# Kernel tuning notes

Hardware: AMD Instinct MI355X
Metric: run time of the kernel (lower is better)

Reference implementation:

```python
import jax, jax.numpy as jnp
import numpy as np

N_NODES = 50000
N_EDGES = 400000
IN_NODE = 16
OUT_NODE = 20
IN_EDGE = 10
HIDDEN_EDGE = 64
HIDDEN_ACTOR = 256
N_ACTIONS = 16
N_GRAPHS = 128
BN_EPS = 1e-5


def setup_inputs() -> dict:
    key = jax.random.key(0)
    ks = jax.random.split(key, 16)
    inp = {
        "x": jax.random.normal(ks[0], (N_NODES, IN_NODE), dtype=jnp.float32),
        "edge_index": jax.random.randint(ks[1], (2, N_EDGES), 0, N_NODES, dtype=jnp.int64),
        "edge_attr": jax.random.normal(ks[2], (N_EDGES, IN_EDGE), dtype=jnp.float32),
        "batch": jnp.sort(jax.random.randint(ks[3], (N_NODES,), 0, N_GRAPHS, dtype=jnp.int64)),
        # edge-nn params: Lin(in_edge,64) -> BN(64) -> ReLU -> Lin(64, in*out)
        "W1": jax.random.normal(ks[4], (IN_EDGE, HIDDEN_EDGE), dtype=jnp.float32) / np.sqrt(IN_EDGE),
        "b1": jnp.zeros((HIDDEN_EDGE,), dtype=jnp.float32),
        "gamma": jnp.ones((HIDDEN_EDGE,), dtype=jnp.float32),
        "beta": jnp.zeros((HIDDEN_EDGE,), dtype=jnp.float32),
        "W2": jax.random.normal(ks[5], (HIDDEN_EDGE, IN_NODE * OUT_NODE), dtype=jnp.float32) / np.sqrt(HIDDEN_EDGE),
        "b2": jnp.zeros((IN_NODE * OUT_NODE,), dtype=jnp.float32),
        # NNConv root weight + bias
        "root": jax.random.normal(ks[6], (IN_NODE, OUT_NODE), dtype=jnp.float32) / np.sqrt(IN_NODE),
        "bias": jnp.zeros((OUT_NODE,), dtype=jnp.float32),
        # actor MLP: Lin(20,256) -> ReLU -> Lin(256, n_actions)
        "A1": jax.random.normal(ks[7], (OUT_NODE, HIDDEN_ACTOR), dtype=jnp.float32) / np.sqrt(OUT_NODE),
        "ab1": jnp.zeros((HIDDEN_ACTOR,), dtype=jnp.float32),
        "A2": jax.random.normal(ks[8], (HIDDEN_ACTOR, N_ACTIONS), dtype=jnp.float32) / np.sqrt(HIDDEN_ACTOR),
        "ab2": jnp.zeros((N_ACTIONS,), dtype=jnp.float32),
    }
    return inp


def reference(x, edge_index, edge_attr, batch, W1, b1, gamma, beta, W2, b2, root, bias, A1, ab1, A2, ab2):
    # edge nn: Linear -> BatchNorm1d (training-mode batch stats) -> ReLU -> Linear
    h = edge_attr @ W1 + b1                                  # [E, 64]
    mu = jnp.mean(h, axis=0)
    var = jnp.mean((h - mu) ** 2, axis=0)                    # biased var, as BN uses
    h = gamma * (h - mu) * jax.lax.rsqrt(var + BN_EPS) + beta
    h = jax.nn.relu(h)
    w = (h @ W2 + b2).reshape(-1, IN_NODE, OUT_NODE)         # [E, in, out]

    src, dst = edge_index[0], edge_index[1]
    msg = jnp.einsum('ei,eio->eo', x[src], w)                # per-edge matvec, [E, out]
    agg = jax.ops.segment_sum(msg, dst, num_segments=N_NODES)  # scatter-add to targets
    out = agg + x @ root + bias                              # [N, out]

    # global_mean_pool over graphs
    sums = jax.ops.segment_sum(out, batch, num_segments=N_GRAPHS)
    counts = jax.ops.segment_sum(jnp.ones((out.shape[0],), out.dtype), batch, num_segments=N_GRAPHS)
    pooled = sums / jnp.maximum(counts, 1.0)[:, None]        # [G, out]

    a = jax.nn.relu(pooled @ A1 + ab1)
    return a @ A2 + ab2                                      # [G, n_actions]
```

## Files before the change

kernel.cpp:

```cpp
#include <hip/hip_runtime.h>

#define N_NODES   50000
#define N_EDGES   400000
#define IN_NODE   16
#define OUT_NODE  20
#define IN_EDGE   10
#define HE        64
#define HA        256
#define N_ACT     16
#define N_GRAPHS  128
#define BN_EPS    1e-5f
#define HNST      68
#define SPLIT     16

typedef __attribute__((ext_vector_type(8))) short short8v;
typedef __attribute__((ext_vector_type(4))) float f32x4;

__device__ __forceinline__ unsigned short f2bf(float f) {
  unsigned u = __float_as_uint(f);
  u += 0x7fffu + ((u >> 16) & 1u);
  return (unsigned short)(u >> 16);
}
__device__ __forceinline__ float bf2f(short s) {
  return __uint_as_float(((unsigned)(unsigned short)s) << 16);
}

#define DPP_ROR_ADD(v, CTRL)                                                  \
  ((v) + __int_as_float(__builtin_amdgcn_update_dpp(                          \
             0, __float_as_int(v), (CTRL), 0xF, 0xF, true)))
#define ROW_SUM16(v)                                                          \
  do {                                                                        \
    v = DPP_ROR_ADD(v, 0x128);                                                \
    v = DPP_ROR_ADD(v, 0x124);                                                \
    v = DPP_ROR_ADD(v, 0x122);                                                \
    v = DPP_ROR_ADD(v, 0x121);                                                \
  } while (0)

__global__ void zero_k(float* __restrict__ ws) {
  ws[blockIdx.x * 256 + threadIdx.x] = 0.f;
}

__global__ __launch_bounds__(256) void prep_k(const int* __restrict__ ei,
                                              const int* __restrict__ batch,
                                              int* __restrict__ hist) {
  __shared__ int lh[N_GRAPHS];
  const int tid = threadIdx.x;
  if (tid < N_GRAPHS) lh[tid] = 0;
  __syncthreads();
  for (int e = blockIdx.x * 256 + tid; e < N_EDGES; e += 256 * 256)
    atomicAdd(&lh[batch[ei[N_EDGES + e]]], 1);
  __syncthreads();
  if (tid < N_GRAPHS && lh[tid] > 0) atomicAdd(&hist[tid], lh[tid]);
}

__global__ void scan_k(const int* __restrict__ hist, int* __restrict__ bstart,
                       int* __restrict__ cursor) {
  __shared__ int v[N_GRAPHS];
  const int t = threadIdx.x;
  const int h = hist[t];
  v[t] = h;
  __syncthreads();
  for (int off = 1; off < N_GRAPHS; off <<= 1) {
    int y = 0;
    if (t >= off) y = v[t - off];
    __syncthreads();
    v[t] += y;
    __syncthreads();
  }
  bstart[t] = v[t] - h;
  cursor[t] = v[t] - h;
  if (t == N_GRAPHS - 1) bstart[N_GRAPHS] = v[t];
}

__global__ __launch_bounds__(256) void scatter_k(
    const float* __restrict__ ea, const int* __restrict__ ei,
    const int* __restrict__ batch, const float* __restrict__ x,
    int* __restrict__ cursor, unsigned short* __restrict__ exb,
    float* __restrict__ hdr) {
  __shared__ int lh[N_GRAPHS];
  __shared__ int gb[N_GRAPHS];
  __shared__ float red[4][72];
  const int tid = threadIdx.x;

  float cs[10];
  float gm[55];
#pragma unroll
  for (int a = 0; a < 10; ++a) cs[a] = 0.f;
#pragma unroll
  for (int u = 0; u < 55; ++u) gm[u] = 0.f;
  if (tid < N_GRAPHS) lh[tid] = 0;
  __syncthreads();

  int gj[7], lr[7];
#pragma unroll
  for (int j = 0; j < 7; ++j) {
    const int e = blockIdx.x * 256 + tid + j * 65536;
    gj[j] = -1;
    lr[j] = 0;
    if (e < N_EDGES) {
      const int g = batch[ei[N_EDGES + e]];
      gj[j] = g;
      lr[j] = atomicAdd(&lh[g], 1);
    }
  }
  __syncthreads();
  if (tid < N_GRAPHS && lh[tid] > 0)
    gb[tid] = atomicAdd(&cursor[tid], lh[tid]);
  __syncthreads();

#pragma unroll
  for (int j = 0; j < 7; ++j) {
    if (gj[j] < 0) continue;
    const int e = blockIdx.x * 256 + tid + j * 65536;
    const float2* rp = reinterpret_cast<const float2*>(ea + (size_t)e * 10);
    float f[10];
#pragma unroll
    for (int p = 0; p < 5; ++p) {
      const float2 t2 = rp[p];
      f[2 * p] = t2.x;
      f[2 * p + 1] = t2.y;
    }
#pragma unroll
    for (int a = 0; a < 10; ++a) cs[a] += f[a];
    int idx = 0;
#pragma unroll
    for (int a = 0; a < 10; ++a)
#pragma unroll
      for (int b = a; b < 10; ++b) {
        gm[idx] = fmaf(f[a], f[b], gm[idx]);
        ++idx;
      }
    const int s = ei[e];
    const float4* xp = reinterpret_cast<const float4*>(&x[(size_t)s * IN_NODE]);
    const float4 x0 = xp[0], x1 = xp[1], x2 = xp[2], x3 = xp[3];
    unsigned u[16];
    u[0] = f2bf(f[0]) | ((unsigned)f2bf(f[1]) << 16);
    u[1] = f2bf(f[2]) | ((unsigned)f2bf(f[3]) << 16);
    u[2] = f2bf(f[4]) | ((unsigned)f2bf(f[5]) << 16);
    u[3] = f2bf(f[6]) | ((unsigned)f2bf(f[7]) << 16);
    u[4] = f2bf(f[8]) | ((unsigned)f2bf(f[9]) << 16);
    u[5] = 0; u[6] = 0; u[7] = 0;
    u[8]  = f2bf(x0.x) | ((unsigned)f2bf(x0.y) << 16);
    u[9]  = f2bf(x0.z) | ((unsigned)f2bf(x0.w) << 16);
    u[10] = f2bf(x1.x) | ((unsigned)f2bf(x1.y) << 16);
    u[11] = f2bf(x1.z) | ((unsigned)f2bf(x1.w) << 16);
    u[12] = f2bf(x2.x) | ((unsigned)f2bf(x2.y) << 16);
    u[13] = f2bf(x2.z) | ((unsigned)f2bf(x2.w) << 16);
    u[14] = f2bf(x3.x) | ((unsigned)f2bf(x3.y) << 16);
    u[15] = f2bf(x3.z) | ((unsigned)f2bf(x3.w) << 16);
    const int pos = gb[gj[j]] + lr[j];
    int4* dst = reinterpret_cast<int4*>(exb + (size_t)pos * 32);
    dst[0] = int4{(int)u[0], (int)u[1], (int)u[2], (int)u[3]};
    dst[1] = int4{(int)u[4], (int)u[5], (int)u[6], (int)u[7]};
    dst[2] = int4{(int)u[8], (int)u[9], (int)u[10], (int)u[11]};
    dst[3] = int4{(int)u[12], (int)u[13], (int)u[14], (int)u[15]};
  }

#pragma unroll
  for (int v = 0; v < 10; ++v)
#pragma unroll
    for (int off = 1; off < 64; off <<= 1) cs[v] += __shfl_xor(cs[v], off, 64);
#pragma unroll
  for (int u = 0; u < 55; ++u)
#pragma unroll
    for (int off = 1; off < 64; off <<= 1) gm[u] += __shfl_xor(gm[u], off, 64);
  const int lane = tid & 63;
  const int w = tid >> 6;
  if (lane == 0) {
#pragma unroll
    for (int v = 0; v < 10; ++v) red[w][v] = cs[v];
#pragma unroll
    for (int u = 0; u < 55; ++u) red[w][10 + u] = gm[u];
  }
  __syncthreads();
  if (tid < 65) {
    const float s = red[0][tid] + red[1][tid] + red[2][tid] + red[3][tid];
    const int dst = (tid < 10) ? tid : 6 + tid;
    atomicAdd(&hdr[dst], s);
  }
}

__global__ __launch_bounds__(256, 2) void s_kernel(
    const unsigned short* __restrict__ exb, const float* __restrict__ W1g,
    const float* __restrict__ W2g, const float* __restrict__ b2g,
    const float* __restrict__ b1, const float* __restrict__ gamma,
    const float* __restrict__ beta, const float* __restrict__ hdr,
    const int* __restrict__ bstart, float* __restrict__ MSGpart) {
  __shared__ short hnT[2][64 * HNST];
  __shared__ short xT[2][16 * HNST];
  __shared__ float mred[4][OUT_NODE];
  __shared__ float scs[HE], c1s[HE];

  const int tid = threadIdx.x;
  const int lane = tid & 63;
  const int w = tid >> 6;
  const int i_col = lane & 15;
  const int kq = lane >> 4;

  if (tid < HE) {
    const int c = tid;
    float wc[10];
#pragma unroll
    for (int k = 0; k < 10; ++k) wc[k] = W1g[k * HE + c];
    float su = 0.f;
#pragma unroll
    for (int k = 0; k < 10; ++k) su = fmaf(hdr[k], wc[k], su);
    float q = 0.f;
    int idx = 0;
#pragma unroll
    for (int a = 0; a < 10; ++a) {
      q = fmaf(hdr[16 + idx], wc[a] * wc[a], q);
      ++idx;
#pragma unroll
      for (int b = a + 1; b < 10; ++b) {
        q = fmaf(2.f * hdr[16 + idx], wc[a] * wc[b], q);
        ++idx;
      }
    }
    const float b1c = b1[c];
    const float invE = 1.f / (float)N_EDGES;
    const float mu = su * invE + b1c;
    const float Eh2 = (q + 2.f * b1c * su) * invE + b1c * b1c;
    const float var = Eh2 - mu * mu;
    const float sc = gamma[c] * rsqrtf(var + BN_EPS);
    scs[c] = sc;
    c1s[c] = sc * (b1c - mu) + beta[c];
  }
  __syncthreads();

  const int g = blockIdx.x / SPLIT;
  const int pp = blockIdx.x - g * SPLIT;
  const int gs = bstart[g], geE = bstart[g + 1];
  const int cnt = geE - gs;
  const int p0 = gs + (cnt * pp) / SPLIT;
  const int p1 = gs + (cnt * (pp + 1)) / SPLIT;

  short8v w1f[4];
  float scv[4], c1v[4];
#pragma unroll
  for (int nt = 0; nt < 4; ++nt) {
    short8v v;
#pragma unroll
    for (int j = 0; j < 8; ++j) {
      const int k = kq * 8 + j;
      const float f = (k < IN_EDGE) ? W1g[k * HE + nt * 16 + i_col] : 0.f;
      v[j] = (short)f2bf(f);
    }
    w1f[nt] = v;
    scv[nt] = scs[nt * 16 + i_col];
    c1v[nt] = c1s[nt * 16 + i_col];
  }

  f32x4 acc = {0.f, 0.f, 0.f, 0.f};
  float xs = 0.f;

  int p = 0;
  for (int base = p0; base < p1; base += 64) {
    {
      const int er = base + w * 16 + i_col;
      short8v ae;
      if (kq < 2) {
        ae = *reinterpret_cast<const short8v*>(&exb[(size_t)er * 32 + kq * 8]);
      } else {
#pragma unroll
        for (int j = 0; j < 8; ++j) ae[j] = 0;
      }
      const f32x4 zero4 = {0.f, 0.f, 0.f, 0.f};
#pragma unroll
      for (int nt = 0; nt < 4; ++nt) {
        const f32x4 hv = __builtin_amdgcn_mfma_f32_16x16x32_bf16(
            ae, w1f[nt], zero4, 0, 0, 0);
        short4 sv;
        {
          const int e0 = base + w * 16 + kq * 4;
          const float h0 = (e0 + 0 < p1) ? fmaxf(fmaf(hv[0], scv[nt], c1v[nt]), 0.f) : 0.f;
          const float h1 = (e0 + 1 < p1) ? fmaxf(fmaf(hv[1], scv[nt], c1v[nt]), 0.f) : 0.f;
          const float h2 = (e0 + 2 < p1) ? fmaxf(fmaf(hv[2], scv[nt], c1v[nt]), 0.f) : 0.f;
          const float h3 = (e0 + 3 < p1) ? fmaxf(fmaf(hv[3], scv[nt], c1v[nt]), 0.f) : 0.f;
          sv.x = (short)f2bf(h0);
          sv.y = (short)f2bf(h1);
          sv.z = (short)f2bf(h2);
          sv.w = (short)f2bf(h3);
        }
        *reinterpret_cast<short4*>(
            &hnT[p][(nt * 16 + i_col) * HNST + w * 16 + kq * 4]) = sv;
      }
    }
    {
      const int et = tid >> 2, iq = tid & 3;
      const int er = base + et;
      short4 xv = {0, 0, 0, 0};
      if (er < p1)
        xv = *reinterpret_cast<const short4*>(
            &exb[(size_t)er * 32 + 16 + iq * 4]);
      xT[p][(iq * 4 + 0) * HNST + et] = xv.x;
      xT[p][(iq * 4 + 1) * HNST + et] = xv.y;
      xT[p][(iq * 4 + 2) * HNST + et] = xv.z;
      xT[p][(iq * 4 + 3) * HNST + et] = xv.w;
    }
    __syncthreads();
#pragma unroll
    for (int ks = 0; ks < 2; ++ks) {
      const short8v a = *reinterpret_cast<const short8v*>(
          &hnT[p][(w * 16 + i_col) * HNST + ks * 32 + kq * 8]);
      const short8v b = *reinterpret_cast<const short8v*>(
          &xT[p][i_col * HNST + ks * 32 + kq * 8]);
      acc = __builtin_amdgcn_mfma_f32_16x16x32_bf16(a, b, acc, 0, 0, 0);
      if (w == 0) {
#pragma unroll
        for (int j = 0; j < 8; ++j) xs += bf2f(b[j]);
      }
    }
    p ^= 1;
  }

  if (w == 0) {
    xs += __shfl_xor(xs, 16, 64);
    xs += __shfl_xor(xs, 32, 64);
  }
  float po[OUT_NODE];
#pragma unroll
  for (int o = 0; o < OUT_NODE; ++o) po[o] = 0.f;
#pragma unroll
  for (int r = 0; r < 4; ++r) {
    const float* w2p =
        &W2g[(size_t)(w * 16 + kq * 4 + r) * (IN_NODE * OUT_NODE) +
             i_col * OUT_NODE];
#pragma unroll
    for (int o = 0; o < OUT_NODE; ++o) po[o] = fmaf(acc[r], w2p[o], po[o]);
  }
  if (w == 0 && kq == 0) {
    const float* b2p = &b2g[i_col * OUT_NODE];
#pragma unroll
    for (int o = 0; o < OUT_NODE; ++o) po[o] = fmaf(xs, b2p[o], po[o]);
  }
#pragma unroll
  for (int o = 0; o < OUT_NODE; ++o) {
    float s = po[o];
    ROW_SUM16(s);
    s += __shfl_xor(s, 16, 64);
    s += __shfl_xor(s, 32, 64);
    po[o] = s;
  }
  if (lane == 0) {
#pragma unroll
    for (int o = 0; o < OUT_NODE; ++o) mred[w][o] = po[o];
  }
  __syncthreads();
  if (tid < OUT_NODE)
    MSGpart[(size_t)blockIdx.x * OUT_NODE + tid] =
        mred[0][tid] + mred[1][tid] + mred[2][tid] + mred[3][tid];
}

__global__ __launch_bounds__(256) void xsum_k(const float* __restrict__ x,
                                              const int* __restrict__ batch,
                                              float* __restrict__ XN,
                                              float* __restrict__ cnt) {
  __shared__ float xn_l[N_GRAPHS * IN_NODE];
  __shared__ float cnt_l[N_GRAPHS];
  const int tid = threadIdx.x;
  const int lane = tid & 63;
  for (int t = tid; t < N_GRAPHS * IN_NODE; t += 256) xn_l[t] = 0.f;
  if (tid < N_GRAPHS) cnt_l[tid] = 0.f;
  __syncthreads();

  const int n = blockIdx.x * 256 + tid;
  const bool valid = n < N_NODES;
  int g = -1;
  float xf[IN_NODE];
  if (valid) {
    g = batch[n];
    const float4* xp = reinterpret_cast<const float4*>(&x[(size_t)n * IN_NODE]);
    const float4 a0 = xp[0], a1 = xp[1], a2 = xp[2], a3 = xp[3];
    xf[0] = a0.x;  xf[1] = a0.y;  xf[2] = a0.z;  xf[3] = a0.w;
    xf[4] = a1.x;  xf[5] = a1.y;  xf[6] = a1.z;  xf[7] = a1.w;
    xf[8] = a2.x;  xf[9] = a2.y;  xf[10] = a2.z; xf[11] = a2.w;
    xf[12] = a3.x; xf[13] = a3.y; xf[14] = a3.z; xf[15] = a3.w;
  } else {
#pragma unroll
    for (int i = 0; i < IN_NODE; ++i) xf[i] = 0.f;
  }

  const int g0 = __builtin_amdgcn_readfirstlane(g);
  const bool uni = (__ballot(valid && (g == g0)) == 0xFFFFFFFFFFFFFFFFull);

  if (uni) {
#pragma unroll
    for (int i = 0; i < IN_NODE; ++i) {
      float s = xf[i];
      ROW_SUM16(s);
      s += __shfl_xor(s, 16, 64);
      s += __shfl_xor(s, 32, 64);
      xf[i] = s;
    }
    if (lane == 0) {
#pragma unroll
      for (int i = 0; i < IN_NODE; ++i) atomicAdd(&xn_l[g0 * IN_NODE + i], xf[i]);
      atomicAdd(&cnt_l[g0], 64.f);
    }
  } else if (valid) {
#pragma unroll
    for (int i = 0; i < IN_NODE; ++i) atomicAdd(&xn_l[g * IN_NODE + i], xf[i]);
    atomicAdd(&cnt_l[g], 1.f);
  }
  __syncthreads();

  if (tid < N_GRAPHS && cnt_l[tid] != 0.f) atomicAdd(&cnt[tid], cnt_l[tid]);
  for (int t = tid; t < N_GRAPHS * IN_NODE; t += 256) {
    const float v = xn_l[t];
    if (v != 0.f) atomicAdd(&XN[t], v);
  }
}

__global__ __launch_bounds__(256) void fuse_k(
    const float* __restrict__ MSGpart, const float* __restrict__ XN,
    const float* __restrict__ cnt, const float* __restrict__ rootg,
    const float* __restrict__ biasg, const float* __restrict__ A1,
    const float* __restrict__ ab1, const float* __restrict__ A2,
    const float* __restrict__ ab2, float* __restrict__ out) {
  __shared__ float pooled[OUT_NODE];
  __shared__ float a_s[HA];
  __shared__ float red[16][N_ACT];

  const int g = blockIdx.x;
  const int tid = threadIdx.x;
  if (tid < OUT_NODE) {
    float s = 0.f;
#pragma unroll
    for (int q = 0; q < SPLIT; ++q)
      s += MSGpart[(size_t)(g * SPLIT + q) * OUT_NODE + tid];
#pragma unroll
    for (int i = 0; i < IN_NODE; ++i)
      s = fmaf(XN[g * IN_NODE + i], rootg[i * OUT_NODE + tid], s);
    const float invc = 1.f / fmaxf(cnt[g], 1.f);
    pooled[tid] = s * invc + biasg[tid];
  }
  __syncthreads();

  {
    float v = ab1[tid];
#pragma unroll
    for (int k = 0; k < OUT_NODE; ++k) v = fmaf(pooled[k], A1[k * HA + tid], v);
    a_s[tid] = fmaxf(v, 0.f);
  }
  __syncthreads();
  {
    const int j = tid & 15, seg = tid >> 4;
    float v = 0.f;
#pragma unroll
    for (int kk = 0; kk < 16; ++kk) {
      const int k = seg * 16 + kk;
      v += a_s[k] * A2[k * N_ACT + j];
    }
    red[seg][j] = v;
  }
  __syncthreads();
  if (tid < N_ACT) {
    float s = ab2[tid];
#pragma unroll
    for (int seg = 0; seg < 16; ++seg) s += red[seg][tid];
    out[g * N_ACT + tid] = s;
  }
}

extern "C" void kernel_launch(void* const* d_in, const int* in_sizes, int n_in,
                              void* d_out, int out_size, void* d_ws,
                              size_t ws_size, hipStream_t stream) {
  const float* x     = (const float*)d_in[0];
  const int*   ei    = (const int*)d_in[1];
  const float* ea    = (const float*)d_in[2];
  const int*   batch = (const int*)d_in[3];
  const float* W1    = (const float*)d_in[4];
  const float* b1    = (const float*)d_in[5];
  const float* gamma = (const float*)d_in[6];
  const float* beta  = (const float*)d_in[7];
  const float* W2    = (const float*)d_in[8];
  const float* b2    = (const float*)d_in[9];
  const float* root  = (const float*)d_in[10];
  const float* bias  = (const float*)d_in[11];
  const float* A1    = (const float*)d_in[12];
  const float* ab1   = (const float*)d_in[13];
  const float* A2    = (const float*)d_in[14];
  const float* ab2   = (const float*)d_in[15];
  float* out = (float*)d_out;

  float* ws = (float*)d_ws;
  int*   iw = (int*)d_ws;
  float* hdr     = ws;
  float* XN      = ws + 256;
  float* cntb    = ws + 2304;
  int*   hist    = iw + 2432;
  int*   bstart  = iw + 2560;
  int*   cursor  = iw + 2696;
  float* MSGpart = ws + 2824;
  unsigned short* exb = (unsigned short*)(iw + 402824);

  zero_k<<<10, 256, 0, stream>>>(ws);
  prep_k<<<256, 256, 0, stream>>>(ei, batch, hist);
  scan_k<<<1, 128, 0, stream>>>(hist, bstart, cursor);
  scatter_k<<<256, 256, 0, stream>>>(ea, ei, batch, x, cursor, exb, hdr);
  s_kernel<<<N_GRAPHS * SPLIT, 256, 0, stream>>>(exb, W1, W2, b2, b1, gamma,
                                                 beta, hdr, bstart, MSGpart);
  xsum_k<<<(N_NODES + 255) / 256, 256, 0, stream>>>(x, batch, XN, cntb);
  fuse_k<<<N_GRAPHS, 256, 0, stream>>>(MSGpart, XN, cntb, root, bias, A1, ab1,
                                       A2, ab2, out);
}
```

Baseline: 84.14 us.

## Replace atomic-cursor edge bucketing with per-block counts and deterministic column scan

Splits the old scatter kernel into a separate edge-attribute Gram-statistics kernel and a counting-sort pipeline. A count kernel writes per-block per-graph histograms and caches each edge's graph id, a column scan computes per-block offsets, and a pack kernel with one edge per thread writes bf16 packed records to their computed slots. This removes the global cursor atomics and the 7-edges-per-thread register-heavy loop and raises parallelism to 1563 blocks. In exchange it adds two more kernel launches and an extra pass over the graph-id array.

```diff
diff --git a/kernel.cpp b/kernel.cpp
--- a/kernel.cpp
+++ b/kernel.cpp
@@ -12,6 +12,7 @@
 #define BN_EPS    1e-5f
 #define HNST      68
 #define SPLIT     16
+#define NB        1563
 
 typedef __attribute__((ext_vector_type(8))) short short8v;
 typedef __attribute__((ext_vector_type(4))) float f32x4;
@@ -40,21 +41,104 @@
   ws[blockIdx.x * 256 + threadIdx.x] = 0.f;
 }
 
-__global__ __launch_bounds__(256) void prep_k(const int* __restrict__ ei,
-                                              const int* __restrict__ batch,
-                                              int* __restrict__ hist) {
+__global__ __launch_bounds__(256) void gram_k(const float* __restrict__ ea,
+                                              float* __restrict__ hdr) {
+  float cs[10];
+  float gm[55];
+#pragma unroll
+  for (int a = 0; a < 10; ++a) cs[a] = 0.f;
+#pragma unroll
+  for (int u = 0; u < 55; ++u) gm[u] = 0.f;
+
+  for (int e = blockIdx.x * 256 + threadIdx.x; e < N_EDGES; e += 256 * 256) {
+    const float2* rp = reinterpret_cast<const float2*>(ea + (size_t)e * 10);
+    float f[10];
+#pragma unroll
+    for (int p = 0; p < 5; ++p) {
+      const float2 t = rp[p];
+      f[2 * p] = t.x;
+      f[2 * p + 1] = t.y;
+    }
+#pragma unroll
+    for (int a = 0; a < 10; ++a) cs[a] += f[a];
+    int idx = 0;
+#pragma unroll
+    for (int a = 0; a < 10; ++a)
+#pragma unroll
+      for (int b = a; b < 10; ++b) {
+        gm[idx] = fmaf(f[a], f[b], gm[idx]);
+        ++idx;
+      }
+  }
+
+#pragma unroll
+  for (int v = 0; v < 10; ++v)
+#pragma unroll
+    for (int off = 1; off < 64; off <<= 1) cs[v] += __shfl_xor(cs[v], off, 64);
+#pragma unroll
+  for (int u = 0; u < 55; ++u)
+#pragma unroll
+    for (int off = 1; off < 64; off <<= 1) gm[u] += __shfl_xor(gm[u], off, 64);
+
+  __shared__ float red[4][72];
+  const int lane = threadIdx.x & 63;
+  const int w = threadIdx.x >> 6;
+  if (lane == 0) {
+#pragma unroll
+    for (int v = 0; v < 10; ++v) red[w][v] = cs[v];
+#pragma unroll
+    for (int u = 0; u < 55; ++u) red[w][10 + u] = gm[u];
+  }
+  __syncthreads();
+  if (threadIdx.x < 65) {
+    const int t = threadIdx.x;
+    const float s = red[0][t] + red[1][t] + red[2][t] + red[3][t];
+    const int dst = (t < 10) ? t : 6 + t;
+    atomicAdd(&hdr[dst], s);
+  }
+}
+
+__global__ __launch_bounds__(256) void count_k(const int* __restrict__ ei,
+                                               const int* __restrict__ batch,
+                                               int* __restrict__ ge,
+                                               int* __restrict__ cnt2dT) {
   __shared__ int lh[N_GRAPHS];
   const int tid = threadIdx.x;
+  const int e = blockIdx.x * 256 + tid;
   if (tid < N_GRAPHS) lh[tid] = 0;
   __syncthreads();
-  for (int e = blockIdx.x * 256 + tid; e < N_EDGES; e += 256 * 256)
-    atomicAdd(&lh[batch[ei[N_EDGES + e]]], 1);
-  __syncthreads();
-  if (tid < N_GRAPHS && lh[tid] > 0) atomicAdd(&hist[tid], lh[tid]);
-}
-
-__global__ void scan_k(const int* __restrict__ hist, int* __restrict__ bstart,
-                       int* __restrict__ cursor) {
+  if (e < N_EDGES) {
+    const int g = batch[ei[N_EDGES + e]];
+    ge[e] = g;
+    atomicAdd(&lh[g], 1);
+  }
+  __syncthreads();
+  if (tid < N_GRAPHS) cnt2dT[tid * NB + blockIdx.x] = lh[tid];
+}
+
+__global__ __launch_bounds__(64) void colscan_k(const int* __restrict__ cnt2dT,
+                                                int* __restrict__ off2dT,
+                                                int* __restrict__ hist) {
+  const int g = blockIdx.x;
+  const int t = threadIdx.x;
+  int running = 0;
+  for (int c = 0; c < (NB + 63) / 64; ++c) {
+    const int b = c * 64 + t;
+    const int v = (b < NB) ? cnt2dT[g * NB + b] : 0;
+    int s = v;
+#pragma unroll
+    for (int off = 1; off < 64; off <<= 1) {
+      const int y = __shfl_up(s, off, 64);
+      if (t >= off) s += y;
+    }
+    if (b < NB) off2dT[g * NB + b] = running + s - v;
+    running += __shfl(s, 63, 64);
+  }
+  if (t == 0) hist[g] = running;
+}
+
+__global__ void scan_k(const int* __restrict__ hist,
+                       int* __restrict__ bstart) {
   __shared__ int v[N_GRAPHS];
   const int t = threadIdx.x;
   const int h = hist[t];
@@ -68,116 +152,64 @@
     __syncthreads();
   }
   bstart[t] = v[t] - h;
-  cursor[t] = v[t] - h;
   if (t == N_GRAPHS - 1) bstart[N_GRAPHS] = v[t];
 }
 
-__global__ __launch_bounds__(256) void scatter_k(
+__global__ __launch_bounds__(256) void scatter_pack_k(
     const float* __restrict__ ea, const int* __restrict__ ei,
-    const int* __restrict__ batch, const float* __restrict__ x,
-    int* __restrict__ cursor, unsigned short* __restrict__ exb,
-    float* __restrict__ hdr) {
+    const int* __restrict__ ge, const float* __restrict__ x,
+    const int* __restrict__ off2dT, const int* __restrict__ bstart,
+    unsigned short* __restrict__ exb) {
   __shared__ int lh[N_GRAPHS];
-  __shared__ int gb[N_GRAPHS];
-  __shared__ float red[4][72];
+  __shared__ int obase[N_GRAPHS];
+  const int b = blockIdx.x;
   const int tid = threadIdx.x;
-
-  float cs[10];
-  float gm[55];
-#pragma unroll
-  for (int a = 0; a < 10; ++a) cs[a] = 0.f;
-#pragma unroll
-  for (int u = 0; u < 55; ++u) gm[u] = 0.f;
+  const int e = b * 256 + tid;
   if (tid < N_GRAPHS) lh[tid] = 0;
   __syncthreads();
-
-  int gj[7], lr[7];
-#pragma unroll
-  for (int j = 0; j < 7; ++j) {
-    const int e = blockIdx.x * 256 + tid + j * 65536;
-    gj[j] = -1;
-    lr[j] = 0;
-    if (e < N_EDGES) {
-      const int g = batch[ei[N_EDGES + e]];
-      gj[j] = g;
-      lr[j] = atomicAdd(&lh[g], 1);
-    }
-  }
-  __syncthreads();
-  if (tid < N_GRAPHS && lh[tid] > 0)
-    gb[tid] = atomicAdd(&cursor[tid], lh[tid]);
-  __syncthreads();
-
-#pragma unroll
-  for (int j = 0; j < 7; ++j) {
-    if (gj[j] < 0) continue;
-    const int e = blockIdx.x * 256 + tid + j * 65536;
-    const float2* rp = reinterpret_cast<const float2*>(ea + (size_t)e * 10);
-    float f[10];
-#pragma unroll
-    for (int p = 0; p < 5; ++p) {
-      const float2 t2 = rp[p];
-      f[2 * p] = t2.x;
-      f[2 * p + 1] = t2.y;
-    }
-#pragma unroll
-    for (int a = 0; a < 10; ++a) cs[a] += f[a];
-    int idx = 0;
-#pragma unroll
-    for (int a = 0; a < 10; ++a)
-#pragma unroll
-      for (int b = a; b < 10; ++b) {
-        gm[idx] = fmaf(f[a], f[b], gm[idx]);
-        ++idx;
-      }
-    const int s = ei[e];
-    const float4* xp = reinterpret_cast<const float4*>(&x[(size_t)s * IN_NODE]);
-    const float4 x0 = xp[0], x1 = xp[1], x2 = xp[2], x3 = xp[3];
-    unsigned u[16];
-    u[0] = f2bf(f[0]) | ((unsigned)f2bf(f[1]) << 16);
-    u[1] = f2bf(f[2]) | ((unsigned)f2bf(f[3]) << 16);
-    u[2] = f2bf(f[4]) | ((unsigned)f2bf(f[5]) << 16);
-    u[3] = f2bf(f[6]) | ((unsigned)f2bf(f[7]) << 16);
-    u[4] = f2bf(f[8]) | ((unsigned)f2bf(f[9]) << 16);
-    u[5] = 0; u[6] = 0; u[7] = 0;
-    u[8]  = f2bf(x0.x) | ((unsigned)f2bf(x0.y) << 16);
-    u[9]  = f2bf(x0.z) | ((unsigned)f2bf(x0.w) << 16);
-    u[10] = f2bf(x1.x) | ((unsigned)f2bf(x1.y) << 16);
-    u[11] = f2bf(x1.z) | ((unsigned)f2bf(x1.w) << 16);
-    u[12] = f2bf(x2.x) | ((unsigned)f2bf(x2.y) << 16);
-    u[13] = f2bf(x2.z) | ((unsigned)f2bf(x2.w) << 16);
-    u[14] = f2bf(x3.x) | ((unsigned)f2bf(x3.y) << 16);
-    u[15] = f2bf(x3.z) | ((unsigned)f2bf(x3.w) << 16);
-    const int pos = gb[gj[j]] + lr[j];
-    int4* dst = reinterpret_cast<int4*>(exb + (size_t)pos * 32);
-    dst[0] = int4{(int)u[0], (int)u[1], (int)u[2], (int)u[3]};
-    dst[1] = int4{(int)u[4], (int)u[5], (int)u[6], (int)u[7]};
-    dst[2] = int4{(int)u[8], (int)u[9], (int)u[10], (int)u[11]};
-    dst[3] = int4{(int)u[12], (int)u[13], (int)u[14], (int)u[15]};
-  }
-
-#pragma unroll
-  for (int v = 0; v < 10; ++v)
-#pragma unroll
-    for (int off = 1; off < 64; off <<= 1) cs[v] += __shfl_xor(cs[v], off, 64);
-#pragma unroll
-  for (int u = 0; u < 55; ++u)
-#pragma unroll
-    for (int off = 1; off < 64; off <<= 1) gm[u] += __shfl_xor(gm[u], off, 64);
-  const int lane = tid & 63;
-  const int w = tid >> 6;
-  if (lane == 0) {
-#pragma unroll
-    for (int v = 0; v < 10; ++v) red[w][v] = cs[v];
-#pragma unroll
-    for (int u = 0; u < 55; ++u) red[w][10 + u] = gm[u];
-  }
-  __syncthreads();
-  if (tid < 65) {
-    const float s = red[0][tid] + red[1][tid] + red[2][tid] + red[3][tid];
-    const int dst = (tid < 10) ? tid : 6 + tid;
-    atomicAdd(&hdr[dst], s);
-  }
+  int g = -1, r = 0;
+  if (e < N_EDGES) {
+    g = ge[e];
+    r = atomicAdd(&lh[g], 1);
+  }
+  if (tid < N_GRAPHS) obase[tid] = bstart[tid] + off2dT[tid * NB + b];
+  __syncthreads();
+  if (e >= N_EDGES) return;
+
+  const float2* rp = reinterpret_cast<const float2*>(ea + (size_t)e * 10);
+  float f[10];
+#pragma unroll
+  for (int p = 0; p < 5; ++p) {
+    const float2 t2 = rp[p];
+    f[2 * p] = t2.x;
+    f[2 * p + 1] = t2.y;
+  }
+  const int s = ei[e];
+  const float4* xp = reinterpret_cast<const float4*>(&x[(size_t)s * IN_NODE]);
+  const float4 x0 = xp[0], x1 = xp[1], x2 = xp[2], x3 = xp[3];
+
+  unsigned u[16];
+  u[0] = f2bf(f[0]) | ((unsigned)f2bf(f[1]) << 16);
+  u[1] = f2bf(f[2]) | ((unsigned)f2bf(f[3]) << 16);
+  u[2] = f2bf(f[4]) | ((unsigned)f2bf(f[5]) << 16);
+  u[3] = f2bf(f[6]) | ((unsigned)f2bf(f[7]) << 16);
+  u[4] = f2bf(f[8]) | ((unsigned)f2bf(f[9]) << 16);
+  u[5] = 0; u[6] = 0; u[7] = 0;
+  u[8]  = f2bf(x0.x) | ((unsigned)f2bf(x0.y) << 16);
+  u[9]  = f2bf(x0.z) | ((unsigned)f2bf(x0.w) << 16);
+  u[10] = f2bf(x1.x) | ((unsigned)f2bf(x1.y) << 16);
+  u[11] = f2bf(x1.z) | ((unsigned)f2bf(x1.w) << 16);
+  u[12] = f2bf(x2.x) | ((unsigned)f2bf(x2.y) << 16);
+  u[13] = f2bf(x2.z) | ((unsigned)f2bf(x2.w) << 16);
+  u[14] = f2bf(x3.x) | ((unsigned)f2bf(x3.y) << 16);
+  u[15] = f2bf(x3.z) | ((unsigned)f2bf(x3.w) << 16);
+
+  const int pos = obase[g] + r;
+  int4* dst = reinterpret_cast<int4*>(exb + (size_t)pos * 32);
+  dst[0] = int4{(int)u[0], (int)u[1], (int)u[2], (int)u[3]};
+  dst[1] = int4{(int)u[4], (int)u[5], (int)u[6], (int)u[7]};
+  dst[2] = int4{(int)u[8], (int)u[9], (int)u[10], (int)u[11]};
+  dst[3] = int4{(int)u[12], (int)u[13], (int)u[14], (int)u[15]};
 }
 
 __global__ __launch_bounds__(256, 2) void s_kernel(
@@ -491,14 +523,18 @@
   float* cntb    = ws + 2304;
   int*   hist    = iw + 2432;
   int*   bstart  = iw + 2560;
-  int*   cursor  = iw + 2696;
   float* MSGpart = ws + 2824;
-  unsigned short* exb = (unsigned short*)(iw + 402824);
+  int*   ge      = iw + 43784;
+  int*   cnt2dT  = iw + 443784;
+  int*   off2dT  = iw + 643848;
+  unsigned short* exb = (unsigned short*)(iw + 843912);
 
   zero_k<<<10, 256, 0, stream>>>(ws);
-  prep_k<<<256, 256, 0, stream>>>(ei, batch, hist);
-  scan_k<<<1, 128, 0, stream>>>(hist, bstart, cursor);
-  scatter_k<<<256, 256, 0, stream>>>(ea, ei, batch, x, cursor, exb, hdr);
+  gram_k<<<256, 256, 0, stream>>>(ea, hdr);
+  count_k<<<NB, 256, 0, stream>>>(ei, batch, ge, cnt2dT);
+  colscan_k<<<N_GRAPHS, 64, 0, stream>>>(cnt2dT, off2dT, hist);
+  scan_k<<<1, 128, 0, stream>>>(hist, bstart);
+  scatter_pack_k<<<NB, 256, 0, stream>>>(ea, ei, ge, x, off2dT, bstart, exb);
   s_kernel<<<N_GRAPHS * SPLIT, 256, 0, stream>>>(exb, W1, W2, b2, b1, gamma,
                                                  beta, hdr, bstart, MSGpart);
   xsum_k<<<(N_NODES + 255) / 256, 256, 0, stream>>>(x, batch, XN, cntb);
```

After: 98.18 us. +16.7%, slower.
